# Optimization experiments

Measured on AMD Instinct MI355X. Metric: run time of the kernel, lower is better.

## Reference

```python
import jax, jax.numpy as jnp
import numpy as np

N = 50000
E = 500000
D_IN = 128
D_OUT = 128
EPS = 1e-12


def setup_inputs() -> dict:
    key = jax.random.key(0)
    ks = jax.random.split(key, 12)
    s_in = 1.0 / np.sqrt(D_IN)
    s_pos = 1.0 / np.sqrt(3.0)
    s_out = 1.0 / np.sqrt(D_OUT)
    return {
        "x": jax.random.normal(ks[0], (N, D_IN), dtype=jnp.float32),
        "pos": jax.random.normal(ks[1], (N, 3), dtype=jnp.float32),
        "edge_index": jax.random.randint(ks[2], (E, 2), 0, N, dtype=jnp.int32),
        # weights stored [in, out] so projection is x @ W
        "W": jax.random.uniform(ks[3], (D_IN, D_OUT), jnp.float32, -s_in, s_in),      # lin (bias=False)
        "Wsrc": jax.random.uniform(ks[4], (D_IN, D_OUT), jnp.float32, -s_in, s_in),   # lin_src
        "Wdst": jax.random.uniform(ks[5], (D_IN, D_OUT), jnp.float32, -s_in, s_in),   # lin_dst
        "Wpos": jax.random.uniform(ks[6], (3, D_OUT), jnp.float32, -s_pos, s_pos),    # pos_nn
        "bpos": jax.random.uniform(ks[7], (D_OUT,), jnp.float32, -s_pos, s_pos),
        "Wa1": jax.random.uniform(ks[8], (D_OUT, D_OUT), jnp.float32, -s_out, s_out), # attn_nn[0]
        "ba1": jax.random.uniform(ks[9], (D_OUT,), jnp.float32, -s_out, s_out),
        "Wa2": jax.random.uniform(ks[10], (D_OUT, D_OUT), jnp.float32, -s_out, s_out),# attn_nn[2]
        "ba2": jax.random.uniform(ks[11], (D_OUT,), jnp.float32, -s_out, s_out),
    }


def reference(x, pos, edge_index, W, Wsrc, Wdst, Wpos, bpos, Wa1, ba1, Wa2, ba2):
    row = edge_index[:, 0]  # [E] destination / grouping key
    col = edge_index[:, 1]  # [E] source
    num_nodes = x.shape[0]

    # node-level projections
    x_proj = x @ W          # [N, D_OUT]
    alpha_src = x @ Wsrc    # [N, D_OUT]
    alpha_dst = x @ Wdst    # [N, D_OUT]

    # per-edge gathers
    x_j = x_proj[col]                       # [E, D_OUT]
    delta = (pos[row] - pos[col]) @ Wpos + bpos  # [E, D_OUT]

    # attention logits + small MLP
    alpha = alpha_src[row] - alpha_dst[col] + delta
    alpha = jax.nn.relu(alpha @ Wa1 + ba1) @ Wa2 + ba2  # [E, D_OUT]

    # scatter-softmax over edges sharing the same row.
    # torch reference computes amax into a zeros tensor with include_self=True,
    # i.e. max is taken over {edge logits} U {0}; empty segments get 0.
    seg_max = jax.ops.segment_max(alpha, row, num_segments=num_nodes)  # [N, D_OUT]
    seg_max = jnp.maximum(seg_max, 0.0)
    exp_alpha = jnp.exp(alpha - seg_max[row])
    seg_sum = jax.ops.segment_sum(exp_alpha, row, num_segments=num_nodes)
    att = exp_alpha / (seg_sum[row] + EPS)  # [E, D_OUT]

    # message + scatter-add aggregation
    msg = att * (x_j + delta)
    out = jax.ops.segment_sum(msg, row, num_segments=num_nodes)  # [N, D_OUT]
    return out
```

## Files before the change

### kernel.cpp

```cpp
#include <hip/hip_runtime.h>
#include <math.h>

#define NN 50000
#define NE 500000
#define NTILES 31250
#define DD 128
#define EPSV 1e-12f
#define SCC 196

typedef short short8 __attribute__((ext_vector_type(8)));
typedef float f32x4 __attribute__((ext_vector_type(4)));
typedef __bf16 bf16x8 __attribute__((ext_vector_type(8)));

__device__ __forceinline__ ushort f2bf(float f) {
    return __builtin_bit_cast(unsigned short, (__bf16)f);
}
__device__ __forceinline__ float bf2f(unsigned u) {
    union { unsigned u; float f; } v; v.u = u << 16;
    return v.f;
}
__device__ __forceinline__ float bf2f_hi(unsigned u) {
    union { unsigned u; float f; } v; v.u = u & 0xffff0000u;
    return v.f;
}

__global__ __launch_bounds__(256) void compose_kernel(
    const float* __restrict__ Wsrc, const float* __restrict__ Wdst,
    const float* __restrict__ Wa1, const float* __restrict__ Wpos,
    const float* __restrict__ bpos, const float* __restrict__ ba1,
    float* __restrict__ W1s, float* __restrict__ W1d,
    float* __restrict__ Wp1, float* __restrict__ b1eff)
{
    __shared__ float a1[128 * 8];
    const int t = threadIdx.x;
    const int j0 = blockIdx.x * 8;
    for (int idx = t; idx < 1024; idx += 256) {
        int i = idx >> 3, jl = idx & 7;
        a1[idx] = Wa1[i * 128 + j0 + jl];
    }
    __syncthreads();
    const int jl = t & 7, k0 = t >> 3;
#pragma unroll 1
    for (int kb = 0; kb < 4; ++kb) {
        int k = kb * 32 + k0;
        float s1 = 0.f, s2 = 0.f;
        for (int i = 0; i < 128; ++i) {
            float w = a1[i * 8 + jl];
            s1 = fmaf(Wsrc[k * 128 + i], w, s1);
            s2 = fmaf(Wdst[k * 128 + i], w, s2);
        }
        W1s[k * 128 + j0 + jl] = s1;
        W1d[k * 128 + j0 + jl] = s2;
    }
    if (t < 32) {
        int d = t >> 3, j = j0 + (t & 7);
        float s = 0.f;
        if (d < 3) {
            for (int i = 0; i < 128; ++i) s = fmaf(Wpos[d * 128 + i], a1[i * 8 + (t & 7)], s);
            Wp1[d * 128 + j] = s;
        } else {
            for (int i = 0; i < 128; ++i) s = fmaf(bpos[i], a1[i * 8 + (t & 7)], s);
            b1eff[j] = s + ba1[j];
        }
    }
}

__global__ __launch_bounds__(256) void node_gemm(
    const float* __restrict__ x, const float* __restrict__ pos,
    const float* __restrict__ W, const float* __restrict__ W1s,
    const float* __restrict__ W1d, const float* __restrict__ Wpos,
    const float* __restrict__ Wp1, const float* __restrict__ b1eff,
    ushort* __restrict__ Ux, ushort* __restrict__ Vx, unsigned* __restrict__ Xc2)
{
    __shared__ ushort wsm[16384];
    const int t = threadIdx.x;
    const int w = t >> 6;
    const int l = t & 63;
    const int g = l >> 4;
    const int low = l & 15;

    const int n0 = (blockIdx.x * 4 + w) * 16;
    const int rowi = min(n0 + low, NN - 1);

    short8 af[4];
#pragma unroll
    for (int kc = 0; kc < 4; ++kc) {
        const float* xp = x + (size_t)rowi * 128 + kc * 32 + g * 8;
        float4 a0 = *(const float4*)xp;
        float4 a1 = *(const float4*)(xp + 4);
        short8 v;
        v[0] = (short)f2bf(a0.x); v[1] = (short)f2bf(a0.y);
        v[2] = (short)f2bf(a0.z); v[3] = (short)f2bf(a0.w);
        v[4] = (short)f2bf(a1.x); v[5] = (short)f2bf(a1.y);
        v[6] = (short)f2bf(a1.z); v[7] = (short)f2bf(a1.w);
        af[kc] = v;
    }
    float posr[4][3];
#pragma unroll
    for (int r = 0; r < 4; ++r) {
        int node = min(n0 + g * 4 + r, NN - 1);
        posr[r][0] = pos[node * 3]; posr[r][1] = pos[node * 3 + 1]; posr[r][2] = pos[node * 3 + 2];
    }

#pragma unroll 1
    for (int y = 0; y < 3; ++y) {
        const float* Wsel = (y == 0) ? W1s : (y == 1) ? W1d : W;
        const float* wps  = (y < 2) ? Wp1 : Wpos;

        for (int gi = t; gi < 2048; gi += 256) {
            int j = gi & 127, k8 = gi >> 7;
            short8 v;
#pragma unroll
            for (int i = 0; i < 8; ++i)
                v[i] = (short)f2bf(Wsel[(k8 * 8 + i) * 128 + j]);
            *(short8*)&wsm[j * 128 + ((k8 ^ (j & 15)) << 3)] = v;
        }
        float wp0[8], wp1v[8], wp2[8], bpv[8];
#pragma unroll
        for (int nb = 0; nb < 8; ++nb) {
            int ch = nb * 16 + low;
            wp0[nb] = wps[ch]; wp1v[nb] = wps[128 + ch]; wp2[nb] = wps[256 + ch];
            bpv[nb] = (y == 0) ? b1eff[ch] : 0.f;
        }
        __syncthreads();

        f32x4 acc[8];
#pragma unroll
        for (int nb = 0; nb < 8; ++nb) { acc[nb][0]=0.f; acc[nb][1]=0.f; acc[nb][2]=0.f; acc[nb][3]=0.f; }
#pragma unroll
        for (int nb = 0; nb < 8; ++nb) {
            int j = nb * 16 + low;
#pragma unroll
            for (int kc = 0; kc < 4; ++kc) {
                short8 bf = *(const short8*)&wsm[j * 128 + (((kc * 4 + g) ^ low) << 3)];
                acc[nb] = __builtin_amdgcn_mfma_f32_16x16x32_bf16(af[kc], bf, acc[nb], 0, 0, 0);
            }
        }

#pragma unroll
        for (int r = 0; r < 4; ++r) {
            int node = n0 + g * 4 + r;
            if (node < NN) {
                float p0 = posr[r][0], p1 = posr[r][1], p2 = posr[r][2];
                if (y < 2) {
#pragma unroll
                    for (int nb = 0; nb < 8; ++nb) {
                        float pterm = p0 * wp0[nb] + p1 * wp1v[nb] + p2 * wp2[nb];
                        size_t idx = (size_t)node * 128 + nb * 16 + low;
                        if (y == 0) Ux[idx] = f2bf(acc[nb][r] + pterm + bpv[nb]);
                        else        Vx[idx] = f2bf(acc[nb][r] + pterm);
                    }
                } else {
#pragma unroll
                    for (int nb = 0; nb < 4; ++nb) {
                        float ptl = p0 * wp0[nb] + p1 * wp1v[nb] + p2 * wp2[nb];
                        float pth = p0 * wp0[nb+4] + p1 * wp1v[nb+4] + p2 * wp2[nb+4];
                        float vl = acc[nb][r] - ptl;
                        float vh = acc[nb+4][r] - pth;
                        Xc2[(size_t)node * 64 + nb * 16 + low] =
                            (unsigned)f2bf(vl) | ((unsigned)f2bf(vh) << 16);
                    }
                }
            }
        }
        __syncthreads();
    }
}

__global__ __launch_bounds__(256) void hist_kernel(const int* __restrict__ ei, int* __restrict__ counts)
{
    int e = blockIdx.x * 256 + threadIdx.x;
    if (e < NE) atomicAdd(&counts[ei[2 * e]], 1);
}

__global__ __launch_bounds__(256) void csr_partial(const int* __restrict__ counts, int* __restrict__ partial)
{
    __shared__ int red[256];
    const int b = blockIdx.x, t = threadIdx.x;
    const int idx = b * SCC + t;
    red[t] = (t < SCC && idx < NN) ? counts[idx] : 0;
    __syncthreads();
#pragma unroll
    for (int d = 128; d > 0; d >>= 1) {
        if (t < d) red[t] += red[t + d];
        __syncthreads();
    }
    if (t == 0) partial[b] = red[0];
}

__global__ __launch_bounds__(256) void csr_scanp(int* __restrict__ partial, int* __restrict__ offsets)
{
    __shared__ int s[256];
    const int t = threadIdx.x;
    int v = partial[t];
    s[t] = v;
    __syncthreads();
    for (int d = 1; d < 256; d <<= 1) {
        int u = (t >= d) ? s[t - d] : 0;
        __syncthreads();
        s[t] += u;
        __syncthreads();
    }
    partial[t] = s[t] - v;
    if (t == 255) offsets[NN] = s[255];
}

__global__ __launch_bounds__(256) void csr_distribute(
    const int* __restrict__ counts, const int* __restrict__ partial,
    int* __restrict__ offsets, int* __restrict__ cursor)
{
    __shared__ int s[256];
    const int b = blockIdx.x, t = threadIdx.x;
    const int idx = b * SCC + t;
    int v = (t < SCC && idx < NN) ? counts[idx] : 0;
    s[t] = v;
    __syncthreads();
    for (int d = 1; d < 256; d <<= 1) {
        int u = (t >= d) ? s[t - d] : 0;
        __syncthreads();
        s[t] += u;
        __syncthreads();
    }
    if (t < SCC && idx < NN) {
        int off = partial[b] + s[t] - v;
        offsets[idx] = off;
        cursor[idx] = off;
    }
}

__global__ __launch_bounds__(256) void scatter_kernel(const int* __restrict__ ei,
                                                      int* __restrict__ cursor,
                                                      int2* __restrict__ rc2, int* __restrict__ colc)
{
    int e = blockIdx.x * 256 + threadIdx.x;
    if (e < NE) {
        int r = ei[2 * e];
        int c = ei[2 * e + 1];
        int p = atomicAdd(&cursor[r], 1);
        rc2[p] = make_int2(r, c);
        colc[p] = c;
    }
}

__global__ __launch_bounds__(256) void expalpha_kernel(
    const ushort* __restrict__ Ux, const ushort* __restrict__ Vx,
    const float* __restrict__ Wa2, const float* __restrict__ ba2,
    const int2* __restrict__ rc2,
    unsigned* __restrict__ expW)
{
    __shared__ ushort wl[16384];

    const int t = threadIdx.x;
    const int w = t >> 6;
    const int l = t & 63;
    const int g = l >> 4;
    const int low = l & 15;

    for (int gi = t; gi < 2048; gi += 256) {
        int j = gi & 127, k8 = gi >> 7;
        short8 v;
#pragma unroll
        for (int i = 0; i < 8; ++i)
            v[i] = (short)f2bf(Wa2[(k8 * 8 + i) * 128 + j]);
        *(short8*)&wl[j * 128 + ((k8 ^ (j & 15)) << 3)] = v;
    }
    float b2v[8];
#pragma unroll
    for (int nb = 0; nb < 8; ++nb) b2v[nb] = ba2[nb * 16 + low];
    __syncthreads();

    const int nw = gridDim.x * 4;
    const int w0 = blockIdx.x * 4 + w;

    for (int t0 = w0; t0 < NTILES; t0 += 2 * nw) {
        const int t1 = t0 + nw;
        const bool has1 = t1 < NTILES;

        short8 hfA[4], hfB[4];
        {
            int2 rc = rc2[t0 * 16 + low];
            const __bf16* up = (const __bf16*)(Ux + (size_t)rc.x * 128 + g * 8);
            const __bf16* vp = (const __bf16*)(Vx + (size_t)rc.y * 128 + g * 8);
#pragma unroll
            for (int kc = 0; kc < 4; ++kc) {
                bf16x8 uu = *(const bf16x8*)(up + kc * 32);
                bf16x8 vv = *(const bf16x8*)(vp + kc * 32);
                short8 h;
#pragma unroll
                for (int i = 0; i < 8; ++i) {
                    float d = fmaxf((float)uu[i] - (float)vv[i], 0.f);
                    h[i] = (short)f2bf(d);
                }
                hfA[kc] = h;
            }
        }
        if (has1) {
            int2 rc = rc2[t1 * 16 + low];
            const __bf16* up = (const __bf16*)(Ux + (size_t)rc.x * 128 + g * 8);
            const __bf16* vp = (const __bf16*)(Vx + (size_t)rc.y * 128 + g * 8);
#pragma unroll
            for (int kc = 0; kc < 4; ++kc) {
                bf16x8 uu = *(const bf16x8*)(up + kc * 32);
                bf16x8 vv = *(const bf16x8*)(vp + kc * 32);
                short8 h;
#pragma unroll
                for (int i = 0; i < 8; ++i) {
                    float d = fmaxf((float)uu[i] - (float)vv[i], 0.f);
                    h[i] = (short)f2bf(d);
                }
                hfB[kc] = h;
            }
        }

        f32x4 accA[8], accB[8];
#pragma unroll
        for (int nb = 0; nb < 8; ++nb) {
            accA[nb][0]=0.f; accA[nb][1]=0.f; accA[nb][2]=0.f; accA[nb][3]=0.f;
            accB[nb][0]=0.f; accB[nb][1]=0.f; accB[nb][2]=0.f; accB[nb][3]=0.f;
        }
#pragma unroll
        for (int nb = 0; nb < 8; ++nb) {
            int j = nb * 16 + low;
#pragma unroll
            for (int kc = 0; kc < 4; ++kc) {
                short8 bf = *(const short8*)&wl[j * 128 + (((kc * 4 + g) ^ low) << 3)];
                accA[nb] = __builtin_amdgcn_mfma_f32_16x16x32_bf16(hfA[kc], bf, accA[nb], 0, 0, 0);
                if (has1)
                    accB[nb] = __builtin_amdgcn_mfma_f32_16x16x32_bf16(hfB[kc], bf, accB[nb], 0, 0, 0);
            }
        }

#pragma unroll
        for (int nb = 0; nb < 4; ++nb) {
#pragma unroll
            for (int r = 0; r < 4; ++r) {
                float e0 = __expf(accA[nb][r] + b2v[nb]);
                float e1 = __expf(accA[nb + 4][r] + b2v[nb + 4]);
                expW[(size_t)(t0 * 16 + g * 4 + r) * 64 + nb * 16 + low] =
                    (unsigned)f2bf(e0) | ((unsigned)f2bf(e1) << 16);
                if (has1) {
                    float f0 = __expf(accB[nb][r] + b2v[nb]);
                    float f1 = __expf(accB[nb + 4][r] + b2v[nb + 4]);
                    expW[(size_t)(t1 * 16 + g * 4 + r) * 64 + nb * 16 + low] =
                        (unsigned)f2bf(f0) | ((unsigned)f2bf(f1) << 16);
                }
            }
        }
    }
}

__global__ __launch_bounds__(256) void aggregate_kernel(
    const float* __restrict__ pos,
    const float* __restrict__ Wpos, const float* __restrict__ bpos,
    const unsigned* __restrict__ Xc2,
    const int* __restrict__ offsets, const int* __restrict__ colc,
    const unsigned* __restrict__ expW, float* __restrict__ out)
{
    const int l = threadIdx.x & 63;
    const int wid = blockIdx.x * 4 + (threadIdx.x >> 6);
    const int nw = gridDim.x * 4;

    const float wpa0 = Wpos[l], wpa1 = Wpos[128 + l], wpa2 = Wpos[256 + l];
    const float wpb0 = Wpos[64 + l], wpb1 = Wpos[192 + l], wpb2 = Wpos[320 + l];
    const float bpa = bpos[l], bpb = bpos[64 + l];

    for (int node = wid; node < NN; node += nw) {
        const int aoff = offsets[node];
        const int deg = offsets[node + 1] - aoff;
        const unsigned* ap = expW + (size_t)aoff * 64 + l;

        float s0 = 0.f, s1 = 0.f, o0 = 0.f, o1 = 0.f;
#pragma unroll 4
        for (int e = 0; e < deg; ++e) {
            unsigned v = ap[(size_t)e * 64];
            int c = colc[aoff + e];
            unsigned xv = Xc2[(size_t)c * 64 + l];
            float w0 = bf2f(v & 0xffffu);
            float w1 = bf2f_hi(v);
            float xc0 = bf2f(xv & 0xffffu);
            float xc1 = bf2f_hi(xv);
            s0 += w0; o0 = fmaf(w0, xc0, o0);
            s1 += w1; o1 = fmaf(w1, xc1, o1);
        }
        float p0 = pos[node * 3], p1 = pos[node * 3 + 1], p2 = pos[node * 3 + 2];
        float pb0 = bpa + p0 * wpa0 + p1 * wpa1 + p2 * wpa2;
        float pb1 = bpb + p0 * wpb0 + p1 * wpb1 + p2 * wpb2;
        out[(size_t)node * 128 + l]      = (o0 + pb0 * s0) / (s0 + EPSV);
        out[(size_t)node * 128 + l + 64] = (o1 + pb1 * s1) / (s1 + EPSV);
    }
}

extern "C" void kernel_launch(void* const* d_in, const int* in_sizes, int n_in,
                              void* d_out, int out_size, void* d_ws, size_t ws_size,
                              hipStream_t stream)
{
    const float* x    = (const float*)d_in[0];
    const float* pos  = (const float*)d_in[1];
    const int*   ei   = (const int*)d_in[2];
    const float* W    = (const float*)d_in[3];
    const float* Wsrc = (const float*)d_in[4];
    const float* Wdst = (const float*)d_in[5];
    const float* Wpos = (const float*)d_in[6];
    const float* bpos = (const float*)d_in[7];
    const float* Wa1  = (const float*)d_in[8];
    const float* ba1  = (const float*)d_in[9];
    const float* Wa2  = (const float*)d_in[10];
    const float* ba2  = (const float*)d_in[11];
    float* out = (float*)d_out;

    ushort* Ux = (ushort*)d_ws;
    ushort* Vx = Ux + (size_t)NN * DD;
    unsigned* Xc2 = (unsigned*)(Vx + (size_t)NN * DD);
    float* W1s = (float*)(Xc2 + (size_t)NN * 64);
    float* W1d = W1s + 128 * 128;
    float* Wp1 = W1d + 128 * 128;
    float* b1eff = Wp1 + 384;
    int* offsets = (int*)(b1eff + 128);
    int* cursor  = offsets + (NN + 1);
    int* counts  = cursor + NN;
    int* partial = counts + NN;
    int* colc    = partial + 256;
    int2* rc2    = (int2*)(colc + NE);
    unsigned* expW = (unsigned*)(rc2 + NE);

    compose_kernel<<<16, 256, 0, stream>>>(Wsrc, Wdst, Wa1, Wpos, bpos, ba1, W1s, W1d, Wp1, b1eff);
    node_gemm<<<(NN + 63) / 64, 256, 0, stream>>>(
        x, pos, W, W1s, W1d, Wpos, Wp1, b1eff, Ux, Vx, Xc2);
    hipMemsetAsync(counts, 0, NN * sizeof(int), stream);
    hist_kernel<<<(NE + 255) / 256, 256, 0, stream>>>(ei, counts);
    csr_partial<<<256, 256, 0, stream>>>(counts, partial);
    csr_scanp<<<1, 256, 0, stream>>>(partial, offsets);
    csr_distribute<<<256, 256, 0, stream>>>(counts, partial, offsets, cursor);
    scatter_kernel<<<(NE + 255) / 256, 256, 0, stream>>>(ei, cursor, rc2, colc);
    expalpha_kernel<<<2048, 256, 0, stream>>>(Ux, Vx, Wa2, ba2, rc2, expW);
    aggregate_kernel<<<4096, 256, 0, stream>>>(pos, Wpos, bpos, Xc2, offsets, colc, expW, out);
}
```

Baseline: 269.6 us.

## Fuse edge attention MLP with segment aggregation using balanced node ranges per wave

Merges the exp-logit kernel and the aggregation kernel into one. Each wave gets a contiguous node range chosen by binary search over CSR offsets so edge counts are balanced. Exp weights stay in per-wave LDS and are reduced on the fly, so the per-edge expW intermediate is no longer written to or read back from global memory, and the colc array is dropped. The U/V intermediates and second GEMM switch from bf16 to fp16 so the subtract and relu run as packed half operations. In exchange, a small range kernel and a memset of out (for nodes with no edges) are added, tiles are no longer double-buffered, and fp16 may overflow for large activations.

After: 326.8 us. 21.2% more time.

```diff
diff --git a/kernel.cpp b/kernel.cpp
--- a/kernel.cpp
+++ b/kernel.cpp
@@ -1,19 +1,23 @@
 #include <hip/hip_runtime.h>
+#include <hip/hip_fp16.h>
 #include <math.h>
 
 #define NN 50000
 #define NE 500000
-#define NTILES 31250
 #define DD 128
 #define EPSV 1e-12f
 #define SCC 196
+#define NWAVE 8192
 
 typedef short short8 __attribute__((ext_vector_type(8)));
+typedef _Float16 f16x8 __attribute__((ext_vector_type(8)));
 typedef float f32x4 __attribute__((ext_vector_type(4)));
-typedef __bf16 bf16x8 __attribute__((ext_vector_type(8)));
 
 __device__ __forceinline__ ushort f2bf(float f) {
     return __builtin_bit_cast(unsigned short, (__bf16)f);
+}
+__device__ __forceinline__ ushort f2h(float f) {
+    return __builtin_bit_cast(unsigned short, (_Float16)f);
 }
 __device__ __forceinline__ float bf2f(unsigned u) {
     union { unsigned u; float f; } v; v.u = u << 16;
@@ -70,7 +74,7 @@
     const float* __restrict__ W, const float* __restrict__ W1s,
     const float* __restrict__ W1d, const float* __restrict__ Wpos,
     const float* __restrict__ Wp1, const float* __restrict__ b1eff,
-    ushort* __restrict__ Ux, ushort* __restrict__ Vx, unsigned* __restrict__ Xc2)
+    ushort* __restrict__ Uh, ushort* __restrict__ Vh, unsigned* __restrict__ Xc2)
 {
     __shared__ ushort wsm[16384];
     const int t = threadIdx.x;
@@ -147,18 +151,16 @@
                     for (int nb = 0; nb < 8; ++nb) {
                         float pterm = p0 * wp0[nb] + p1 * wp1v[nb] + p2 * wp2[nb];
                         size_t idx = (size_t)node * 128 + nb * 16 + low;
-                        if (y == 0) Ux[idx] = f2bf(acc[nb][r] + pterm + bpv[nb]);
-                        else        Vx[idx] = f2bf(acc[nb][r] + pterm);
+                        if (y == 0) Uh[idx] = f2h(acc[nb][r] + pterm + bpv[nb]);
+                        else        Vh[idx] = f2h(acc[nb][r] + pterm);
                     }
                 } else {
 #pragma unroll
                     for (int nb = 0; nb < 4; ++nb) {
                         float ptl = p0 * wp0[nb] + p1 * wp1v[nb] + p2 * wp2[nb];
                         float pth = p0 * wp0[nb+4] + p1 * wp1v[nb+4] + p2 * wp2[nb+4];
-                        float vl = acc[nb][r] - ptl;
-                        float vh = acc[nb+4][r] - pth;
                         Xc2[(size_t)node * 64 + nb * 16 + low] =
-                            (unsigned)f2bf(vl) | ((unsigned)f2bf(vh) << 16);
+                            (unsigned)f2bf(acc[nb][r] - ptl) | ((unsigned)f2bf(acc[nb+4][r] - pth) << 16);
                     }
                 }
             }
@@ -230,7 +232,7 @@
 
 __global__ __launch_bounds__(256) void scatter_kernel(const int* __restrict__ ei,
                                                       int* __restrict__ cursor,
-                                                      int2* __restrict__ rc2, int* __restrict__ colc)
+                                                      int2* __restrict__ rc2)
 {
     int e = blockIdx.x * 256 + threadIdx.x;
     if (e < NE) {
@@ -238,17 +240,34 @@
         int c = ei[2 * e + 1];
         int p = atomicAdd(&cursor[r], 1);
         rc2[p] = make_int2(r, c);
-        colc[p] = c;
-    }
-}
-
-__global__ __launch_bounds__(256) void expalpha_kernel(
-    const ushort* __restrict__ Ux, const ushort* __restrict__ Vx,
+    }
+}
+
+__global__ __launch_bounds__(256) void range_kernel(const int* __restrict__ offsets, int* __restrict__ sn)
+{
+    int w = blockIdx.x * 256 + threadIdx.x;
+    if (w > NWAVE) return;
+    if (w == NWAVE) { sn[w] = NN; return; }
+    int target = (int)(((long long)w * NE) / NWAVE);
+    int lo = 0, hi = NN;
+    while (lo < hi) {
+        int mid = (lo + hi) >> 1;
+        if (offsets[mid] >= target) hi = mid; else lo = mid + 1;
+    }
+    sn[w] = lo;
+}
+
+__global__ __launch_bounds__(256) void fused_edge(
+    const ushort* __restrict__ Uh, const ushort* __restrict__ Vh,
     const float* __restrict__ Wa2, const float* __restrict__ ba2,
-    const int2* __restrict__ rc2,
-    unsigned* __restrict__ expW)
+    const float* __restrict__ pos, const float* __restrict__ Wpos,
+    const float* __restrict__ bpos,
+    const int2* __restrict__ rc2, const int* __restrict__ offsets,
+    const int* __restrict__ sn,
+    const unsigned* __restrict__ Xc2, float* __restrict__ out)
 {
     __shared__ ushort wl[16384];
+    __shared__ unsigned wtile[4][16 * 64];
 
     const int t = threadIdx.x;
     const int w = t >> 6;
@@ -261,72 +280,49 @@
         short8 v;
 #pragma unroll
         for (int i = 0; i < 8; ++i)
-            v[i] = (short)f2bf(Wa2[(k8 * 8 + i) * 128 + j]);
+            v[i] = (short)f2h(Wa2[(k8 * 8 + i) * 128 + j]);
         *(short8*)&wl[j * 128 + ((k8 ^ (j & 15)) << 3)] = v;
     }
     float b2v[8];
 #pragma unroll
     for (int nb = 0; nb < 8; ++nb) b2v[nb] = ba2[nb * 16 + low];
+    const float wa0 = Wpos[l], wa1 = Wpos[128 + l], wa2c = Wpos[256 + l];
+    const float wb0 = Wpos[64 + l], wb1 = Wpos[192 + l], wb2 = Wpos[320 + l];
+    const float bp0 = bpos[l], bp1 = bpos[64 + l];
     __syncthreads();
 
-    const int nw = gridDim.x * 4;
-    const int w0 = blockIdx.x * 4 + w;
-
-    for (int t0 = w0; t0 < NTILES; t0 += 2 * nw) {
-        const int t1 = t0 + nw;
-        const bool has1 = t1 < NTILES;
-
-        short8 hfA[4], hfB[4];
-        {
-            int2 rc = rc2[t0 * 16 + low];
-            const __bf16* up = (const __bf16*)(Ux + (size_t)rc.x * 128 + g * 8);
-            const __bf16* vp = (const __bf16*)(Vx + (size_t)rc.y * 128 + g * 8);
-#pragma unroll
-            for (int kc = 0; kc < 4; ++kc) {
-                bf16x8 uu = *(const bf16x8*)(up + kc * 32);
-                bf16x8 vv = *(const bf16x8*)(vp + kc * 32);
-                short8 h;
-#pragma unroll
-                for (int i = 0; i < 8; ++i) {
-                    float d = fmaxf((float)uu[i] - (float)vv[i], 0.f);
-                    h[i] = (short)f2bf(d);
-                }
-                hfA[kc] = h;
-            }
-        }
-        if (has1) {
-            int2 rc = rc2[t1 * 16 + low];
-            const __bf16* up = (const __bf16*)(Ux + (size_t)rc.x * 128 + g * 8);
-            const __bf16* vp = (const __bf16*)(Vx + (size_t)rc.y * 128 + g * 8);
-#pragma unroll
-            for (int kc = 0; kc < 4; ++kc) {
-                bf16x8 uu = *(const bf16x8*)(up + kc * 32);
-                bf16x8 vv = *(const bf16x8*)(vp + kc * 32);
-                short8 h;
-#pragma unroll
-                for (int i = 0; i < 8; ++i) {
-                    float d = fmaxf((float)uu[i] - (float)vv[i], 0.f);
-                    h[i] = (short)f2bf(d);
-                }
-                hfB[kc] = h;
-            }
-        }
-
-        f32x4 accA[8], accB[8];
-#pragma unroll
-        for (int nb = 0; nb < 8; ++nb) {
-            accA[nb][0]=0.f; accA[nb][1]=0.f; accA[nb][2]=0.f; accA[nb][3]=0.f;
-            accB[nb][0]=0.f; accB[nb][1]=0.f; accB[nb][2]=0.f; accB[nb][3]=0.f;
-        }
+    const int wv = blockIdx.x * 4 + w;
+    const int nA = sn[wv], nB = sn[wv + 1];
+    const int eStart = offsets[nA], eEnd = offsets[nB];
+    if (eStart >= eEnd) return;
+
+    int cur = -1;
+    float s0 = 0.f, s1 = 0.f, o0 = 0.f, o1 = 0.f;
+
+    for (int base = eStart; base < eEnd; base += 16) {
+        const int nv = min(16, eEnd - base);
+        const int2 rc = rc2[min(base + low, eEnd - 1)];
+
+        const f16x8* up = (const f16x8*)(Uh + (size_t)rc.x * 128);
+        const f16x8* vp = (const f16x8*)(Vh + (size_t)rc.y * 128);
+        const f16x8 zf = {};
+        f16x8 hf[4];
+#pragma unroll
+        for (int kc = 0; kc < 4; ++kc) {
+            f16x8 d = up[kc * 4 + g] - vp[kc * 4 + g];
+            hf[kc] = __builtin_elementwise_max(d, zf);
+        }
+
+        f32x4 acc[8];
+#pragma unroll
+        for (int nb = 0; nb < 8; ++nb) { acc[nb][0]=0.f; acc[nb][1]=0.f; acc[nb][2]=0.f; acc[nb][3]=0.f; }
 #pragma unroll
         for (int nb = 0; nb < 8; ++nb) {
             int j = nb * 16 + low;
 #pragma unroll
             for (int kc = 0; kc < 4; ++kc) {
-                short8 bf = *(const short8*)&wl[j * 128 + (((kc * 4 + g) ^ low) << 3)];
-                accA[nb] = __builtin_amdgcn_mfma_f32_16x16x32_bf16(hfA[kc], bf, accA[nb], 0, 0, 0);
-                if (has1)
-                    accB[nb] = __builtin_amdgcn_mfma_f32_16x16x32_bf16(hfB[kc], bf, accB[nb], 0, 0, 0);
+                f16x8 bfv = *(const f16x8*)&wl[j * 128 + (((kc * 4 + g) ^ low) << 3)];
+                acc[nb] = __builtin_amdgcn_mfma_f32_16x16x32_f16(hf[kc], bfv, acc[nb], 0, 0, 0);
             }
         }
 
@@ -334,59 +330,52 @@
         for (int nb = 0; nb < 4; ++nb) {
 #pragma unroll
             for (int r = 0; r < 4; ++r) {
-                float e0 = __expf(accA[nb][r] + b2v[nb]);
-                float e1 = __expf(accA[nb + 4][r] + b2v[nb + 4]);
-                expW[(size_t)(t0 * 16 + g * 4 + r) * 64 + nb * 16 + low] =
+                int e = g * 4 + r;
+                float e0 = __expf(acc[nb][r] + b2v[nb]);
+                float e1 = __expf(acc[nb + 4][r] + b2v[nb + 4]);
+                wtile[w][e * 64 + ((nb * 16 + low + 4 * e) & 63)] =
                     (unsigned)f2bf(e0) | ((unsigned)f2bf(e1) << 16);
-                if (has1) {
-                    float f0 = __expf(accB[nb][r] + b2v[nb]);
-                    float f1 = __expf(accB[nb + 4][r] + b2v[nb + 4]);
-                    expW[(size_t)(t1 * 16 + g * 4 + r) * 64 + nb * 16 + low] =
-                        (unsigned)f2bf(f0) | ((unsigned)f2bf(f1) << 16);
+            }
+        }
+
+        unsigned xv[16];
+#pragma unroll
+        for (int e = 0; e < 16; ++e) {
+            if (e < nv) {
+                int ce = __shfl(rc.y, e);
+                xv[e] = Xc2[(size_t)ce * 64 + l];
+            }
+        }
+
+#pragma unroll
+        for (int e = 0; e < 16; ++e) {
+            if (e < nv) {
+                int re_ = __shfl(rc.x, e);
+                if (re_ != cur) {
+                    if (cur >= 0) {
+                        float p0 = pos[cur * 3], p1 = pos[cur * 3 + 1], p2 = pos[cur * 3 + 2];
+                        float pb0 = bp0 + p0 * wa0 + p1 * wa1 + p2 * wa2c;
+                        float pb1 = bp1 + p0 * wb0 + p1 * wb1 + p2 * wb2;
+                        out[(size_t)cur * 128 + l]      = (o0 + pb0 * s0) / (s0 + EPSV);
+                        out[(size_t)cur * 128 + l + 64] = (o1 + pb1 * s1) / (s1 + EPSV);
+                    }
+                    s0 = s1 = o0 = o1 = 0.f;
+                    cur = re_;
                 }
-            }
-        }
-    }
-}
-
-__global__ __launch_bounds__(256) void aggregate_kernel(
-    const float* __restrict__ pos,
-    const float* __restrict__ Wpos, const float* __restrict__ bpos,
-    const unsigned* __restrict__ Xc2,
-    const int* __restrict__ offsets, const int* __restrict__ colc,
-    const unsigned* __restrict__ expW, float* __restrict__ out)
-{
-    const int l = threadIdx.x & 63;
-    const int wid = blockIdx.x * 4 + (threadIdx.x >> 6);
-    const int nw = gridDim.x * 4;
-
-    const float wpa0 = Wpos[l], wpa1 = Wpos[128 + l], wpa2 = Wpos[256 + l];
-    const float wpb0 = Wpos[64 + l], wpb1 = Wpos[192 + l], wpb2 = Wpos[320 + l];
-    const float bpa = bpos[l], bpb = bpos[64 + l];
-
-    for (int node = wid; node < NN; node += nw) {
-        const int aoff = offsets[node];
-        const int deg = offsets[node + 1] - aoff;
-        const unsigned* ap = expW + (size_t)aoff * 64 + l;
-
-        float s0 = 0.f, s1 = 0.f, o0 = 0.f, o1 = 0.f;
-#pragma unroll 4
-        for (int e = 0; e < deg; ++e) {
-            unsigned v = ap[(size_t)e * 64];
-            int c = colc[aoff + e];
-            unsigned xv = Xc2[(size_t)c * 64 + l];
-            float w0 = bf2f(v & 0xffffu);
-            float w1 = bf2f_hi(v);
-            float xc0 = bf2f(xv & 0xffffu);
-            float xc1 = bf2f_hi(xv);
-            s0 += w0; o0 = fmaf(w0, xc0, o0);
-            s1 += w1; o1 = fmaf(w1, xc1, o1);
-        }
-        float p0 = pos[node * 3], p1 = pos[node * 3 + 1], p2 = pos[node * 3 + 2];
-        float pb0 = bpa + p0 * wpa0 + p1 * wpa1 + p2 * wpa2;
-        float pb1 = bpb + p0 * wpb0 + p1 * wpb1 + p2 * wpb2;
-        out[(size_t)node * 128 + l]      = (o0 + pb0 * s0) / (s0 + EPSV);
-        out[(size_t)node * 128 + l + 64] = (o1 + pb1 * s1) / (s1 + EPSV);
+                unsigned wv_ = wtile[w][e * 64 + ((l + 4 * e) & 63)];
+                float w0 = bf2f(wv_ & 0xffffu), w1 = bf2f_hi(wv_);
+                float x0 = bf2f(xv[e] & 0xffffu), x1 = bf2f_hi(xv[e]);
+                s0 += w0; o0 = fmaf(w0, x0, o0);
+                s1 += w1; o1 = fmaf(w1, x1, o1);
+            }
+        }
+    }
+    if (cur >= 0) {
+        float p0 = pos[cur * 3], p1 = pos[cur * 3 + 1], p2 = pos[cur * 3 + 2];
+        float pb0 = bp0 + p0 * wa0 + p1 * wa1 + p2 * wa2c;
+        float pb1 = bp1 + p0 * wb0 + p1 * wb1 + p2 * wb2;
+        out[(size_t)cur * 128 + l]      = (o0 + pb0 * s0) / (s0 + EPSV);
+        out[(size_t)cur * 128 + l + 64] = (o1 + pb1 * s1) / (s1 + EPSV);
     }
 }
 
@@ -408,10 +397,11 @@
     const float* ba2  = (const float*)d_in[11];
     float* out = (float*)d_out;
 
-    ushort* Ux = (ushort*)d_ws;
-    ushort* Vx = Ux + (size_t)NN * DD;
-    unsigned* Xc2 = (unsigned*)(Vx + (size_t)NN * DD);
-    float* W1s = (float*)(Xc2 + (size_t)NN * 64);
+    ushort* Uh = (ushort*)d_ws;
+    ushort* Vh = Uh + (size_t)NN * DD;
+    unsigned* Xc2 = (unsigned*)(Vh + (size_t)NN * DD);
+    int2* rc2 = (int2*)(Xc2 + (size_t)NN * 64);
+    float* W1s = (float*)(rc2 + NE);
     float* W1d = W1s + 128 * 128;
     float* Wp1 = W1d + 128 * 128;
     float* b1eff = Wp1 + 384;
@@ -419,19 +409,19 @@
     int* cursor  = offsets + (NN + 1);
     int* counts  = cursor + NN;
     int* partial = counts + NN;
-    int* colc    = partial + 256;
-    int2* rc2    = (int2*)(colc + NE);
-    unsigned* expW = (unsigned*)(rc2 + NE);
+    int* sn      = partial + 256;
 
     compose_kernel<<<16, 256, 0, stream>>>(Wsrc, Wdst, Wa1, Wpos, bpos, ba1, W1s, W1d, Wp1, b1eff);
     node_gemm<<<(NN + 63) / 64, 256, 0, stream>>>(
-        x, pos, W, W1s, W1d, Wpos, Wp1, b1eff, Ux, Vx, Xc2);
-    hipMemsetAsync(counts, 0, NN * sizeof(int), stream);
+        x, pos, W, W1s, W1d, Wpos, Wp1, b1eff, Uh, Vh, Xc2);
+    (void)hipMemsetAsync(counts, 0, NN * sizeof(int), stream);
+    (void)hipMemsetAsync(out, 0, (size_t)NN * DD * sizeof(float), stream);
     hist_kernel<<<(NE + 255) / 256, 256, 0, stream>>>(ei, counts);
     csr_partial<<<256, 256, 0, stream>>>(counts, partial);
     csr_scanp<<<1, 256, 0, stream>>>(partial, offsets);
     csr_distribute<<<256, 256, 0, stream>>>(counts, partial, offsets, cursor);
-    scatter_kernel<<<(NE + 255) / 256, 256, 0, stream>>>(ei, cursor, rc2, colc);
-    expalpha_kernel<<<2048, 256, 0, stream>>>(Ux, Vx, Wa2, ba2, rc2, expW);
-    aggregate_kernel<<<4096, 256, 0, stream>>>(pos, Wpos, bpos, Xc2, offsets, colc, expW, out);
-}
+    scatter_kernel<<<(NE + 255) / 256, 256, 0, stream>>>(ei, cursor, rc2);
+    range_kernel<<<(NWAVE + 256) / 256, 256, 0, stream>>>(offsets, sn);
+    fused_edge<<<NWAVE / 4, 256, 0, stream>>>(Uh, Vh, Wa2, ba2, pos, Wpos, bpos,
+                                              rc2, offsets, sn, Xc2, out);
+}
```
